# Performance work log

Hardware: AMD Instinct MI355X
Metric: run time of the kernel (lower is better)

## Reference

```python
import jax, jax.numpy as jnp
import numpy as np
from jax import lax

B, L = 2, 5000            # images, candidate lines per image
C_IN, C_LOI = 256, 128    # backbone channels, dim_loi
H = W = 256               # feature-map spatial size (indices clamped to 255)
N_PTS0, N_PTS1 = 32, 8    # points sampled per line, after maxpool
POOL = N_PTS0 // N_PTS1   # MaxPool1d kernel/stride = 4
PLANES = C_LOI // 2       # Bottleneck1D mid channels
EPS = 1e-5


def setup_inputs() -> dict:
    key = jax.random.key(0)
    ks = jax.random.split(key, 16)
    f32 = jnp.float32
    s = 0.05
    feature = jax.random.normal(ks[0], (B, C_IN, H, W), f32)
    lines = jax.random.uniform(ks[1], (B, L, 2, 2), f32, minval=0.0, maxval=255.0)
    return {
        "feature": feature,
        "lines": lines,
        "fc1_w": jax.random.normal(ks[2], (C_LOI, C_IN), f32) * s,
        "fc1_b": jnp.zeros((C_LOI,), f32),
        "bn1_g": jnp.ones((C_LOI,), f32),
        "bn1_b": jnp.zeros((C_LOI,), f32),
        "bn1_m": jax.random.normal(ks[3], (C_LOI,), f32) * 0.1,
        "bn1_v": jax.random.uniform(ks[4], (C_LOI,), f32, minval=0.5, maxval=1.5),
        "conv1_w": jax.random.normal(ks[5], (PLANES, C_LOI), f32) * s,
        "conv1_b": jnp.zeros((PLANES,), f32),
        "bn2_g": jnp.ones((PLANES,), f32),
        "bn2_b": jnp.zeros((PLANES,), f32),
        "bn2_m": jax.random.normal(ks[6], (PLANES,), f32) * 0.1,
        "bn2_v": jax.random.uniform(ks[7], (PLANES,), f32, minval=0.5, maxval=1.5),
        "conv2_w": jax.random.normal(ks[8], (PLANES, PLANES, 3), f32) * s,
        "conv2_b": jnp.zeros((PLANES,), f32),
        "bn3_g": jnp.ones((PLANES,), f32),
        "bn3_b": jnp.zeros((PLANES,), f32),
        "bn3_m": jax.random.normal(ks[9], (PLANES,), f32) * 0.1,
        "bn3_v": jax.random.uniform(ks[10], (PLANES,), f32, minval=0.5, maxval=1.5),
        "conv3_w": jax.random.normal(ks[11], (C_LOI, PLANES), f32) * s,
        "conv3_b": jnp.zeros((C_LOI,), f32),
        "fc2_w": jax.random.normal(ks[12], (3, C_LOI * N_PTS1), f32) * s,
        "fc2_b": jnp.zeros((3,), f32),
    }


def _bn(x, g, b, m, v):
    # eval-mode BatchNorm1d over [N, C, T]
    inv = g / jnp.sqrt(v + EPS)
    return x * inv[None, :, None] + (b - m * inv)[None, :, None]


def _bilinear_sample(feat, lines):
    # feat: [B, C, H, W], lines: [B, L, 2, 2] -> [B, L, C, N_PTS0]
    lam = jnp.linspace(0.0, 1.0, N_PTS0, dtype=feat.dtype)[:, None]  # [P,1]
    # p = lam * endpoint0 + (1-lam) * endpoint1 - 0.5  -> [B, L, P, 2]
    p = lines[:, :, 0:1, :] * lam + lines[:, :, 1:2, :] * (1.0 - lam) - 0.5
    px, py = p[..., 0], p[..., 1]                       # [B, L, P]
    px0 = jnp.clip(jnp.floor(px), 0.0, 255.0)
    py0 = jnp.clip(jnp.floor(py), 0.0, 255.0)
    px1 = jnp.clip(px0 + 1.0, 0.0, 255.0)
    py1 = jnp.clip(py0 + 1.0, 0.0, 255.0)
    ix0, iy0 = px0.astype(jnp.int32), py0.astype(jnp.int32)
    ix1, iy1 = px1.astype(jnp.int32), py1.astype(jnp.int32)
    w00 = (px1 - px) * (py1 - py)
    w10 = (px - px0) * (py1 - py)
    w01 = (px1 - px) * (py - py0)
    w11 = (px - px0) * (py - py0)

    def one_image(f, a0, b0, a1, b1, c00, c10, c01, c11):
        # f: [C,H,W], indices/weights: [L,P] -> [C,L,P]
        return (f[:, a0, b0] * c00 + f[:, a1, b0] * c10 +
                f[:, a0, b1] * c01 + f[:, a1, b1] * c11)

    xp = jax.vmap(one_image)(feat, ix0, iy0, ix1, iy1, w00, w10, w01, w11)
    return jnp.transpose(xp, (0, 2, 1, 3))  # [B, L, C, P]


def _forward(feature, lines, fc1_w, fc1_b, bn1_g, bn1_b, bn1_m, bn1_v,
             conv1_w, conv1_b, bn2_g, bn2_b, bn2_m, bn2_v,
             conv2_w, conv2_b, bn3_g, bn3_b, bn3_m, bn3_v,
             conv3_w, conv3_b, fc2_w, fc2_b):
    # fc1: 1x1 conv over the backbone feature map
    x = jnp.einsum('oc,bchw->bohw', fc1_w, feature) + fc1_b[None, :, None, None]
    xp = _bilinear_sample(x, lines)                     # [B, L, C_LOI, P]
    xp = xp.reshape(B * L, C_LOI, N_PTS0)
    # MaxPool1d(kernel=POOL, stride=POOL)
    xp = xp.reshape(B * L, C_LOI, N_PTS1, POOL).max(axis=-1)  # [N, C, T]
    # Bottleneck1D residual branch: BN-ReLU-Conv1(k1)-BN-ReLU-Conv(k3)-BN-ReLU-Conv(k1)
    h = jax.nn.relu(_bn(xp, bn1_g, bn1_b, bn1_m, bn1_v))
    h = jnp.einsum('oc,nct->not', conv1_w, h) + conv1_b[None, :, None]
    h = jax.nn.relu(_bn(h, bn2_g, bn2_b, bn2_m, bn2_v))
    h = lax.conv_general_dilated(h, conv2_w, window_strides=(1,),
                                 padding=((1, 1),),
                                 dimension_numbers=('NCH', 'OIH', 'NCH'))
    h = h + conv2_b[None, :, None]
    h = jax.nn.relu(_bn(h, bn3_g, bn3_b, bn3_m, bn3_v))
    h = jnp.einsum('oc,nct->not', conv3_w, h) + conv3_b[None, :, None]
    xp = xp + h
    # fc2: ReLU + Linear(dim_loi * n_pts1 -> 3)
    flat = jax.nn.relu(xp).reshape(B * L, C_LOI * N_PTS1)
    return flat @ fc2_w.T + fc2_b


def reference(feature, lines, fc1_w, fc1_b, bn1_g, bn1_b, bn1_m, bn1_v,
              conv1_w, conv1_b, bn2_g, bn2_b, bn2_m, bn2_v,
              conv2_w, conv2_b, bn3_g, bn3_b, bn3_m, bn3_v,
              conv3_w, conv3_b, fc2_w, fc2_b):
    return _forward(feature, lines, fc1_w, fc1_b, bn1_g, bn1_b, bn1_m, bn1_v,
                    conv1_w, conv1_b, bn2_g, bn2_b, bn2_m, bn2_v,
                    conv2_w, conv2_b, bn3_g, bn3_b, bn3_m, bn3_v,
                    conv3_w, conv3_b, fc2_w, fc2_b)
```

## Files before the change

kernel.cpp:

```cpp
#include <hip/hip_runtime.h>
#include <hip/hip_bf16.h>

#define BB 2
#define LL 5000
#define CIN 256
#define CLOI 128
#define HH 256
#define WW 256
#define HWP (HH*WW)
#define NPTS0 32
#define NPTS1 8
#define PLANES 64
#define EPSV 1e-5f

#define X_BYTES   ((size_t)BB * HWP * CLOI * 2)
#define XS_BYTES  ((size_t)BB * LL * 1024 * 2)
#define W1S_OFF   (X_BYTES + XS_BYTES)
#define W2S_OFF   (W1S_OFF + 16384)
#define W3S_OFF   (W2S_OFF + 24576)
#define B1P_OFF   (W3S_OFF + 16384)
#define B2P_OFF   (B1P_OFF + 256)
#define S1_OFF    (B2P_OFF + 256)
#define T1_OFF    (S1_OFF + 512)
#define W0S_OFF   (T1_OFF + 512)

typedef unsigned int uint;
typedef unsigned short ushort;
typedef __attribute__((ext_vector_type(8))) short short8;
typedef __attribute__((ext_vector_type(4))) float f32x4;

__device__ __forceinline__ float bf2f(ushort u) {
    uint v = ((uint)u) << 16;
    return __uint_as_float(v);
}
__device__ __forceinline__ ushort f2bf(float f) {
    uint x = __float_as_uint(f);
    uint r = (x + 0x7fffu + ((x >> 16) & 1u)) >> 16;
    return (ushort)r;
}
__device__ __forceinline__ uint pack2(float a, float b) {
    return (uint)f2bf(a) | ((uint)f2bf(b) << 16);
}

__global__ __launch_bounds__(256) void fc1_kernel(
    const float* __restrict__ feature, const ushort* __restrict__ w0s,
    const float* __restrict__ fc1_b, ushort* __restrict__ xout)
{
    __shared__ ushort sF[32 * 64 * 8];

    int tid = threadIdx.x;
    int tile = blockIdx.x;
    int b = tile >> 10;
    int p0 = (tile & 1023) << 6;
    int wv = tid >> 6, lane = tid & 63;
    int q = lane >> 4, ln = lane & 15;

    short8 afr[8][2];
#pragma unroll
    for (int kg = 0; kg < 8; kg++)
#pragma unroll
        for (int mt = 0; mt < 2; mt++)
            afr[kg][mt] = *(const short8*)(w0s + ((size_t)((kg * 4 + q) * 128 + wv * 32 + mt * 16 + ln)) * 8);

    const float* fb = feature + (size_t)b * CIN * HWP + p0;
    int g_ = tid >> 4;
    int qd = tid & 15;
#pragma unroll
    for (int s = 0; s < 2; s++) {
        int g = s * 16 + g_;
        const float* src = fb + (size_t)(g * 8) * HWP + qd * 4;
        float4 rv[8];
#pragma unroll
        for (int j = 0; j < 8; j++) rv[j] = *(const float4*)(src + (size_t)j * HWP);
#pragma unroll
        for (int i = 0; i < 4; i++) {
            uint4 u;
            u.x = pack2(((const float*)&rv[0])[i], ((const float*)&rv[1])[i]);
            u.y = pack2(((const float*)&rv[2])[i], ((const float*)&rv[3])[i]);
            u.z = pack2(((const float*)&rv[4])[i], ((const float*)&rv[5])[i]);
            u.w = pack2(((const float*)&rv[6])[i], ((const float*)&rv[7])[i]);
            *(uint4*)(&sF[(g * 64 + qd * 4 + i) * 8]) = u;
        }
    }
    __syncthreads();

    const f32x4 fzero = { 0.f, 0.f, 0.f, 0.f };
    f32x4 acc[2][4];
#pragma unroll
    for (int mt = 0; mt < 2; mt++)
#pragma unroll
        for (int nt = 0; nt < 4; nt++) acc[mt][nt] = fzero;

#pragma unroll
    for (int kg = 0; kg < 8; kg++) {
#pragma unroll
        for (int nt = 0; nt < 4; nt++) {
            short8 bfr = *(short8*)(&sF[((kg * 4 + q) * 64 + nt * 16 + ln) * 8]);
            acc[0][nt] = __builtin_amdgcn_mfma_f32_16x16x32_bf16(afr[kg][0], bfr, acc[0][nt], 0, 0, 0);
            acc[1][nt] = __builtin_amdgcn_mfma_f32_16x16x32_bf16(afr[kg][1], bfr, acc[1][nt], 0, 0, 0);
        }
    }

    float bias[8];
    *(float4*)bias       = *(const float4*)(fc1_b + wv * 32 + q * 4);
    *(float4*)(bias + 4) = *(const float4*)(fc1_b + wv * 32 + 16 + q * 4);
    ushort* xrow = xout + (size_t)b * HWP * CLOI;
#pragma unroll
    for (int mt = 0; mt < 2; mt++)
#pragma unroll
        for (int nt = 0; nt < 4; nt++) {
            uint2 u;
            u.x = pack2(acc[mt][nt][0] + bias[mt * 4 + 0], acc[mt][nt][1] + bias[mt * 4 + 1]);
            u.y = pack2(acc[mt][nt][2] + bias[mt * 4 + 2], acc[mt][nt][3] + bias[mt * 4 + 3]);
            *(uint2*)(xrow + (size_t)(p0 + nt * 16 + ln) * CLOI + wv * 32 + mt * 16 + q * 4) = u;
        }
}

__global__ __launch_bounds__(256) void prep_kernel(
    const float* __restrict__ conv1_w, const float* __restrict__ conv1_b,
    const float* __restrict__ bn2_g, const float* __restrict__ bn2_b,
    const float* __restrict__ bn2_m, const float* __restrict__ bn2_v,
    const float* __restrict__ conv2_w, const float* __restrict__ conv2_b,
    const float* __restrict__ bn3_g, const float* __restrict__ bn3_b,
    const float* __restrict__ bn3_m, const float* __restrict__ bn3_v,
    const float* __restrict__ conv3_w,
    const float* __restrict__ bn1_g, const float* __restrict__ bn1_b,
    const float* __restrict__ bn1_m, const float* __restrict__ bn1_v,
    const float* __restrict__ fc1_w,
    ushort* __restrict__ w1s, ushort* __restrict__ w2s, ushort* __restrict__ w3s,
    float* __restrict__ b1p, float* __restrict__ b2p,
    float* __restrict__ s1o, float* __restrict__ t1o,
    ushort* __restrict__ w0s)
{
    int idx = blockIdx.x * 256 + threadIdx.x;
    if (idx < 8192) {
        int kg = idx >> 9, rem = idx & 511, m = rem >> 3, j = rem & 7;
        int c = kg * 8 + j;
        float s2 = bn2_g[m] * rsqrtf(bn2_v[m] + EPSV);
        w1s[idx] = f2bf(conv1_w[m * 128 + c] * s2);
    }
    if (idx < 12288) {
        int dt = idx >> 12, rem = idx & 4095;
        int kg = rem >> 9, m = (rem >> 3) & 63, j = rem & 7;
        int i = kg * 8 + j;
        float s3 = bn3_g[m] * rsqrtf(bn3_v[m] + EPSV);
        w2s[idx] = f2bf(conv2_w[m * 192 + i * 3 + dt] * s3);
    }
    if (idx < 8192) {
        int kg = idx >> 10, rem = idx & 1023, m = rem >> 3, j = rem & 7;
        w3s[idx] = f2bf(conv3_w[m * 64 + kg * 8 + j]);
    }
    if (idx < 32768) {
        int grp = idx >> 10, rem = idx & 1023, m = rem >> 3, j = rem & 7;
        w0s[idx] = f2bf(fc1_w[m * CIN + grp * 8 + j]);
    }
    if (idx < 64) {
        float s2 = bn2_g[idx] * rsqrtf(bn2_v[idx] + EPSV);
        b1p[idx] = conv1_b[idx] * s2 + bn2_b[idx] - bn2_m[idx] * s2;
        float s3 = bn3_g[idx] * rsqrtf(bn3_v[idx] + EPSV);
        b2p[idx] = conv2_b[idx] * s3 + bn3_b[idx] - bn3_m[idx] * s3;
    }
    if (idx < 128) {
        float s1 = bn1_g[idx] * rsqrtf(bn1_v[idx] + EPSV);
        s1o[idx] = s1;
        t1o[idx] = bn1_b[idx] - bn1_m[idx] * s1;
    }
}

__global__ __launch_bounds__(256) void sample_kernel(
    const ushort* __restrict__ x, const float* __restrict__ lines,
    ushort* __restrict__ xsb)
{
    __shared__ int   sIdx[NPTS0][4];
    __shared__ float sWt[NPTS0][4];

    int n = blockIdx.x;
    int b = n / LL;
    int tid = threadIdx.x;

    if (tid < NPTS0) {
        int j = tid;
        float lam = (float)j * (1.0f / 31.0f);
        const float* lp = lines + (size_t)n * 4;
        float e0x = lp[0], e0y = lp[1], e1x = lp[2], e1y = lp[3];
        float px = e0x * lam + e1x * (1.f - lam) - 0.5f;
        float py = e0y * lam + e1y * (1.f - lam) - 0.5f;
        float px0 = fminf(fmaxf(floorf(px), 0.f), 255.f);
        float py0 = fminf(fmaxf(floorf(py), 0.f), 255.f);
        float px1 = fminf(px0 + 1.f, 255.f);
        float py1 = fminf(py0 + 1.f, 255.f);
        int ix0 = (int)px0, iy0 = (int)py0, ix1 = (int)px1, iy1 = (int)py1;
        sIdx[j][0] = ix0 * WW + iy0;
        sIdx[j][1] = ix1 * WW + iy0;
        sIdx[j][2] = ix0 * WW + iy1;
        sIdx[j][3] = ix1 * WW + iy1;
        sWt[j][0] = (px1 - px) * (py1 - py);
        sWt[j][1] = (px - px0) * (py1 - py);
        sWt[j][2] = (px1 - px) * (py - py0);
        sWt[j][3] = (px - px0) * (py - py0);
    }
    __syncthreads();

    int w = tid >> 6, lane = tid & 63;
    const uint* xb = (const uint*)(x + (size_t)b * HWP * CLOI);

    float m00 = -INFINITY, m10 = -INFINITY;
    float m01 = -INFINITY, m11 = -INFINITY;

#pragma unroll
    for (int jj = 0; jj < 8; jj++) {
        int j = w * 8 + jj;
        int i00 = sIdx[j][0], i10 = sIdx[j][1], i01 = sIdx[j][2], i11 = sIdx[j][3];
        float w00 = sWt[j][0], w10 = sWt[j][1], w01 = sWt[j][2], w11 = sWt[j][3];
        uint u00 = xb[(size_t)i00 * 64 + lane];
        uint u10 = xb[(size_t)i10 * 64 + lane];
        uint u01 = xb[(size_t)i01 * 64 + lane];
        uint u11 = xb[(size_t)i11 * 64 + lane];
        float v0 = bf2f((ushort)(u00 & 0xffff)) * w00 + bf2f((ushort)(u10 & 0xffff)) * w10
                 + bf2f((ushort)(u01 & 0xffff)) * w01 + bf2f((ushort)(u11 & 0xffff)) * w11;
        float v1 = bf2f((ushort)(u00 >> 16)) * w00 + bf2f((ushort)(u10 >> 16)) * w10
                 + bf2f((ushort)(u01 >> 16)) * w01 + bf2f((ushort)(u11 >> 16)) * w11;
        if (jj < 4) { m00 = fmaxf(m00, v0); m10 = fmaxf(m10, v1); }
        else        { m01 = fmaxf(m01, v0); m11 = fmaxf(m11, v1); }
    }

    ushort* basep = xsb + (size_t)n * 1024;
    int kg = lane >> 2;
    int j2 = (lane & 3) * 2;
    *(uint*)(basep + kg * 64 + (2 * w) * 8 + j2) = pack2(m00, m10);
    *(uint*)(basep + kg * 64 + (2 * w + 1) * 8 + j2) = pack2(m01, m11);
}

__global__ __launch_bounds__(256) void head_kernel(
    const ushort* __restrict__ xsb,
    const ushort* __restrict__ w1s, const ushort* __restrict__ w2s,
    const ushort* __restrict__ w3s,
    const float* __restrict__ b1p, const float* __restrict__ b2p,
    const float* __restrict__ s1g, const float* __restrict__ t1g,
    const float* __restrict__ conv3_b,
    const float* __restrict__ fc2_w, const float* __restrict__ fc2_b,
    float* __restrict__ out)
{
    __shared__ ushort sXS[8192];
    __shared__ ushort sH1[8192];
    __shared__ ushort sB2[4096];
    __shared__ float  sFC2[3072];
    __shared__ float  sS1[128], sT1[128];
    __shared__ float  sB1[64], sB2b[64], sB3b[128];

    int tid = threadIdx.x;
    int wv = tid >> 6, lane = tid & 63;
    int q = lane >> 4, ln = lane & 15;
    int L0 = blockIdx.x * 8;
    int colg = wv * 16 + ln;

    if (tid < 128) { sS1[tid] = s1g[tid]; sT1[tid] = t1g[tid]; sB3b[tid] = conv3_b[tid]; }
    if (tid < 64)  { sB1[tid] = b1p[tid]; sB2b[tid] = b2p[tid]; }
#pragma unroll
    for (int it = 0; it < 12; it++) sFC2[it * 256 + tid] = fc2_w[it * 256 + tid];
    __syncthreads();

#pragma unroll
    for (int it = 0; it < 4; it++) {
        int ch = it * 256 + tid;
        int l = ch >> 7, wc = ch & 127;
        int kg = wc >> 3, tt = wc & 7;
        int col = l * 8 + tt;
        uint4 raw = *(const uint4*)(xsb + (size_t)(L0 + l) * 1024 + wc * 8);
        int off = (kg * 64 + col) * 8;
        *(uint4*)(&sXS[off]) = raw;
        uint rw[4] = { raw.x, raw.y, raw.z, raw.w };
        uint hw[4];
#pragma unroll
        for (int p = 0; p < 4; p++) {
            int c = kg * 8 + p * 2;
            float v0 = bf2f((ushort)(rw[p] & 0xffff));
            float v1 = bf2f((ushort)(rw[p] >> 16));
            float h0 = fmaxf(v0 * sS1[c] + sT1[c], 0.f);
            float h1v = fmaxf(v1 * sS1[c + 1] + sT1[c + 1], 0.f);
            hw[p] = pack2(h0, h1v);
        }
        uint4 hv; hv.x = hw[0]; hv.y = hw[1]; hv.z = hw[2]; hv.w = hw[3];
        *(uint4*)(&sH1[off]) = hv;
    }
    __syncthreads();

    const short8 bzero = { 0, 0, 0, 0, 0, 0, 0, 0 };
    const f32x4 fzero = { 0.f, 0.f, 0.f, 0.f };

    f32x4 acc1[4];
#pragma unroll
    for (int mt = 0; mt < 4; mt++) acc1[mt] = fzero;
#pragma unroll
    for (int ks = 0; ks < 4; ks++) {
        short8 b = *(short8*)(&sH1[((ks * 4 + q) * 64 + colg) * 8]);
#pragma unroll
        for (int mt = 0; mt < 4; mt++) {
            short8 a = *(const short8*)(w1s + ((ks * 4 + q) * 64 + mt * 16 + ln) * 8);
            acc1[mt] = __builtin_amdgcn_mfma_f32_16x16x32_bf16(a, b, acc1[mt], 0, 0, 0);
        }
    }
#pragma unroll
    for (int mt = 0; mt < 4; mt++) {
        int m0 = mt * 16 + q * 4;
        float v0 = fmaxf(acc1[mt][0] + sB1[m0 + 0], 0.f);
        float v1 = fmaxf(acc1[mt][1] + sB1[m0 + 1], 0.f);
        float v2 = fmaxf(acc1[mt][2] + sB1[m0 + 2], 0.f);
        float v3 = fmaxf(acc1[mt][3] + sB1[m0 + 3], 0.f);
        uint2 u; u.x = pack2(v0, v1); u.y = pack2(v2, v3);
        *(uint2*)(&sB2[((m0 >> 3) * 64 + colg) * 8 + (m0 & 7)]) = u;
    }
    __syncthreads();

    f32x4 acc2[4];
#pragma unroll
    for (int mt = 0; mt < 4; mt++) acc2[mt] = fzero;
    int tpos = colg & 7;
#pragma unroll
    for (int dt = 0; dt < 3; dt++) {
        int tsh = tpos + dt - 1;
        bool valid = ((unsigned)tsh < 8u);
        int colr = colg + dt - 1;
        colr = colr < 0 ? 0 : (colr > 63 ? 63 : colr);
#pragma unroll
        for (int ks = 0; ks < 2; ks++) {
            short8 b = *(short8*)(&sB2[((ks * 4 + q) * 64 + colr) * 8]);
            b = valid ? b : bzero;
#pragma unroll
            for (int mt = 0; mt < 4; mt++) {
                short8 a = *(const short8*)(w2s + dt * 4096 + ((ks * 4 + q) * 64 + mt * 16 + ln) * 8);
                acc2[mt] = __builtin_amdgcn_mfma_f32_16x16x32_bf16(a, b, acc2[mt], 0, 0, 0);
            }
        }
    }
#pragma unroll
    for (int mt = 0; mt < 4; mt++) {
        int m0 = mt * 16 + q * 4;
        float v0 = fmaxf(acc2[mt][0] + sB2b[m0 + 0], 0.f);
        float v1 = fmaxf(acc2[mt][1] + sB2b[m0 + 1], 0.f);
        float v2 = fmaxf(acc2[mt][2] + sB2b[m0 + 2], 0.f);
        float v3 = fmaxf(acc2[mt][3] + sB2b[m0 + 3], 0.f);
        uint2 u; u.x = pack2(v0, v1); u.y = pack2(v2, v3);
        *(uint2*)(&sH1[((m0 >> 3) * 64 + colg) * 8 + (m0 & 7)]) = u;
    }
    __syncthreads();

    f32x4 acc3[8];
#pragma unroll
    for (int mt = 0; mt < 8; mt++) acc3[mt] = fzero;
#pragma unroll
    for (int ks = 0; ks < 2; ks++) {
        short8 b = *(short8*)(&sH1[((ks * 4 + q) * 64 + colg) * 8]);
#pragma unroll
        for (int mt = 0; mt < 8; mt++) {
            short8 a = *(const short8*)(w3s + ((ks * 4 + q) * 128 + mt * 16 + ln) * 8);
            acc3[mt] = __builtin_amdgcn_mfma_f32_16x16x32_bf16(a, b, acc3[mt], 0, 0, 0);
        }
    }

    float p0 = 0.f, p1 = 0.f, p2 = 0.f;
#pragma unroll
    for (int mt = 0; mt < 8; mt++) {
#pragma unroll
        for (int r = 0; r < 4; r++) {
            int m = mt * 16 + q * 4 + r;
            float xsv = bf2f(sXS[(m >> 3) * 512 + colg * 8 + (m & 7)]);
            float v = fmaxf(xsv + acc3[mt][r] + sB3b[m], 0.f);
            int fi = m * 8 + tpos;
            p0 += v * sFC2[fi];
            p1 += v * sFC2[1024 + fi];
            p2 += v * sFC2[2048 + fi];
        }
    }
    p0 += __shfl_xor(p0, 32); p1 += __shfl_xor(p1, 32); p2 += __shfl_xor(p2, 32);
    p0 += __shfl_xor(p0, 16); p1 += __shfl_xor(p1, 16); p2 += __shfl_xor(p2, 16);
    p0 += __shfl_xor(p0, 4);  p1 += __shfl_xor(p1, 4);  p2 += __shfl_xor(p2, 4);
    p0 += __shfl_xor(p0, 2);  p1 += __shfl_xor(p1, 2);  p2 += __shfl_xor(p2, 2);
    p0 += __shfl_xor(p0, 1);  p1 += __shfl_xor(p1, 1);  p2 += __shfl_xor(p2, 1);

    if (lane == 0 || lane == 8) {
        int line = L0 + wv * 2 + (lane >> 3);
        out[(size_t)line * 3 + 0] = p0 + fc2_b[0];
        out[(size_t)line * 3 + 1] = p1 + fc2_b[1];
        out[(size_t)line * 3 + 2] = p2 + fc2_b[2];
    }
}

extern "C" void kernel_launch(void* const* d_in, const int* in_sizes, int n_in,
                              void* d_out, int out_size, void* d_ws, size_t ws_size,
                              hipStream_t stream) {
    const float* feature = (const float*)d_in[0];
    const float* lines   = (const float*)d_in[1];
    const float* fc1_w   = (const float*)d_in[2];
    const float* fc1_b   = (const float*)d_in[3];
    const float* bn1_g   = (const float*)d_in[4];
    const float* bn1_b   = (const float*)d_in[5];
    const float* bn1_m   = (const float*)d_in[6];
    const float* bn1_v   = (const float*)d_in[7];
    const float* conv1_w = (const float*)d_in[8];
    const float* conv1_b = (const float*)d_in[9];
    const float* bn2_g   = (const float*)d_in[10];
    const float* bn2_b   = (const float*)d_in[11];
    const float* bn2_m   = (const float*)d_in[12];
    const float* bn2_v   = (const float*)d_in[13];
    const float* conv2_w = (const float*)d_in[14];
    const float* conv2_b = (const float*)d_in[15];
    const float* bn3_g   = (const float*)d_in[16];
    const float* bn3_b   = (const float*)d_in[17];
    const float* bn3_m   = (const float*)d_in[18];
    const float* bn3_v   = (const float*)d_in[19];
    const float* conv3_w = (const float*)d_in[20];
    const float* conv3_b = (const float*)d_in[21];
    const float* fc2_w   = (const float*)d_in[22];
    const float* fc2_b   = (const float*)d_in[23];
    float* out = (float*)d_out;

    char* ws = (char*)d_ws;
    ushort* x_bf = (ushort*)ws;
    ushort* xs_b = (ushort*)(ws + X_BYTES);
    ushort* w1s  = (ushort*)(ws + W1S_OFF);
    ushort* w2s  = (ushort*)(ws + W2S_OFF);
    ushort* w3s  = (ushort*)(ws + W3S_OFF);
    float*  b1p  = (float*)(ws + B1P_OFF);
    float*  b2p  = (float*)(ws + B2P_OFF);
    float*  s1g  = (float*)(ws + S1_OFF);
    float*  t1g  = (float*)(ws + T1_OFF);
    ushort* w0s  = (ushort*)(ws + W0S_OFF);

    prep_kernel<<<128, 256, 0, stream>>>(
        conv1_w, conv1_b, bn2_g, bn2_b, bn2_m, bn2_v,
        conv2_w, conv2_b, bn3_g, bn3_b, bn3_m, bn3_v,
        conv3_w, bn1_g, bn1_b, bn1_m, bn1_v, fc1_w,
        w1s, w2s, w3s, b1p, b2p, s1g, t1g, w0s);
    fc1_kernel<<<2048, 256, 0, stream>>>(feature, w0s, fc1_b, x_bf);
    sample_kernel<<<BB * LL, 256, 0, stream>>>(x_bf, lines, xs_b);
    head_kernel<<<BB * LL / 8, 256, 0, stream>>>(
        xs_b, w1s, w2s, w3s, b1p, b2p, s1g, t1g, conv3_b, fc2_w, fc2_b, out);
}
```

Baseline: 299.3 us.

## Vectorize bilinear gathers, use hardware bf16 packing, drop fc2 LDS staging

```diff
diff --git a/kernel.cpp b/kernel.cpp
--- a/kernel.cpp
+++ b/kernel.cpp
@@ -29,17 +29,20 @@
 typedef __attribute__((ext_vector_type(8))) short short8;
 typedef __attribute__((ext_vector_type(4))) float f32x4;
 
-__device__ __forceinline__ float bf2f(ushort u) {
-    uint v = ((uint)u) << 16;
-    return __uint_as_float(v);
-}
+__device__ __forceinline__ float bfLow(uint u)  { return __uint_as_float(u << 16); }
+__device__ __forceinline__ float bfHigh(uint u) { return __uint_as_float(u & 0xffff0000u); }
+__device__ __forceinline__ float bf2f(ushort u) { return __uint_as_float(((uint)u) << 16); }
 __device__ __forceinline__ ushort f2bf(float f) {
     uint x = __float_as_uint(f);
     uint r = (x + 0x7fffu + ((x >> 16) & 1u)) >> 16;
     return (ushort)r;
 }
-__device__ __forceinline__ uint pack2(float a, float b) {
-    return (uint)f2bf(a) | ((uint)f2bf(b) << 16);
+__device__ __forceinline__ uint pk2(float a, float b) {
+    float2 f; f.x = a; f.y = b;
+    __hip_bfloat162 h = __float22bfloat162_rn(f);
+    uint r;
+    __builtin_memcpy(&r, &h, 4);
+    return r;
 }
 
 __global__ __launch_bounds__(256) void fc1_kernel(
@@ -75,10 +78,10 @@
 #pragma unroll
         for (int i = 0; i < 4; i++) {
             uint4 u;
-            u.x = pack2(((const float*)&rv[0])[i], ((const float*)&rv[1])[i]);
-            u.y = pack2(((const float*)&rv[2])[i], ((const float*)&rv[3])[i]);
-            u.z = pack2(((const float*)&rv[4])[i], ((const float*)&rv[5])[i]);
-            u.w = pack2(((const float*)&rv[6])[i], ((const float*)&rv[7])[i]);
+            u.x = pk2(((const float*)&rv[0])[i], ((const float*)&rv[1])[i]);
+            u.y = pk2(((const float*)&rv[2])[i], ((const float*)&rv[3])[i]);
+            u.z = pk2(((const float*)&rv[4])[i], ((const float*)&rv[5])[i]);
+            u.w = pk2(((const float*)&rv[6])[i], ((const float*)&rv[7])[i]);
             *(uint4*)(&sF[(g * 64 + qd * 4 + i) * 8]) = u;
         }
     }
@@ -110,8 +113,8 @@
 #pragma unroll
         for (int nt = 0; nt < 4; nt++) {
             uint2 u;
-            u.x = pack2(acc[mt][nt][0] + bias[mt * 4 + 0], acc[mt][nt][1] + bias[mt * 4 + 1]);
-            u.y = pack2(acc[mt][nt][2] + bias[mt * 4 + 2], acc[mt][nt][3] + bias[mt * 4 + 3]);
+            u.x = pk2(acc[mt][nt][0] + bias[mt * 4 + 0], acc[mt][nt][1] + bias[mt * 4 + 1]);
+            u.y = pk2(acc[mt][nt][2] + bias[mt * 4 + 2], acc[mt][nt][3] + bias[mt * 4 + 3]);
             *(uint2*)(xrow + (size_t)(p0 + nt * 16 + ln) * CLOI + wv * 32 + mt * 16 + q * 4) = u;
         }
 }
@@ -171,8 +174,8 @@
     const ushort* __restrict__ x, const float* __restrict__ lines,
     ushort* __restrict__ xsb)
 {
-    __shared__ int   sIdx[NPTS0][4];
-    __shared__ float sWt[NPTS0][4];
+    __shared__ int    sBase[NPTS0];
+    __shared__ float4 sW4[NPTS0];
 
     int n = blockIdx.x;
     int b = n / LL;
@@ -187,48 +190,57 @@
         float py = e0y * lam + e1y * (1.f - lam) - 0.5f;
         float px0 = fminf(fmaxf(floorf(px), 0.f), 255.f);
         float py0 = fminf(fmaxf(floorf(py), 0.f), 255.f);
-        float px1 = fminf(px0 + 1.f, 255.f);
-        float py1 = fminf(py0 + 1.f, 255.f);
-        int ix0 = (int)px0, iy0 = (int)py0, ix1 = (int)px1, iy1 = (int)py1;
-        sIdx[j][0] = ix0 * WW + iy0;
-        sIdx[j][1] = ix1 * WW + iy0;
-        sIdx[j][2] = ix0 * WW + iy1;
-        sIdx[j][3] = ix1 * WW + iy1;
-        sWt[j][0] = (px1 - px) * (py1 - py);
-        sWt[j][1] = (px - px0) * (py1 - py);
-        sWt[j][2] = (px1 - px) * (py - py0);
-        sWt[j][3] = (px - px0) * (py - py0);
-    }
-    __syncthreads();
-
-    int w = tid >> 6, lane = tid & 63;
-    const uint* xb = (const uint*)(x + (size_t)b * HWP * CLOI);
-
-    float m00 = -INFINITY, m10 = -INFINITY;
-    float m01 = -INFINITY, m11 = -INFINITY;
+        float px1 = px0 + 1.f;
+        float py1 = py0 + 1.f;
+        int ix0 = (int)px0, iy0 = (int)py0;
+        sBase[j] = (ix0 * WW + iy0) * 256;
+        float4 w;
+        w.x = (px1 - px) * (py1 - py);
+        w.y = (px - px0) * (py1 - py);
+        w.z = (px1 - px) * (py - py0);
+        w.w = (px - px0) * (py - py0);
+        sW4[j] = w;
+    }
+    __syncthreads();
+
+    int wv = tid >> 6, lane = tid & 63;
+    bool hiHalf = lane >= 32;
+    int loff = lane * 8;
+    const char* xbc = (const char*)(x + (size_t)b * HWP * CLOI);
+
+    float m0 = -INFINITY, m1 = -INFINITY, m2 = -INFINITY, m3 = -INFINITY;
 
 #pragma unroll
     for (int jj = 0; jj < 8; jj++) {
-        int j = w * 8 + jj;
-        int i00 = sIdx[j][0], i10 = sIdx[j][1], i01 = sIdx[j][2], i11 = sIdx[j][3];
-        float w00 = sWt[j][0], w10 = sWt[j][1], w01 = sWt[j][2], w11 = sWt[j][3];
-        uint u00 = xb[(size_t)i00 * 64 + lane];
-        uint u10 = xb[(size_t)i10 * 64 + lane];
-        uint u01 = xb[(size_t)i01 * 64 + lane];
-        uint u11 = xb[(size_t)i11 * 64 + lane];
-        float v0 = bf2f((ushort)(u00 & 0xffff)) * w00 + bf2f((ushort)(u10 & 0xffff)) * w10
-                 + bf2f((ushort)(u01 & 0xffff)) * w01 + bf2f((ushort)(u11 & 0xffff)) * w11;
-        float v1 = bf2f((ushort)(u00 >> 16)) * w00 + bf2f((ushort)(u10 >> 16)) * w10
-                 + bf2f((ushort)(u01 >> 16)) * w01 + bf2f((ushort)(u11 >> 16)) * w11;
-        if (jj < 4) { m00 = fmaxf(m00, v0); m10 = fmaxf(m10, v1); }
-        else        { m01 = fmaxf(m01, v0); m11 = fmaxf(m11, v1); }
-    }
-
-    ushort* basep = xsb + (size_t)n * 1024;
-    int kg = lane >> 2;
-    int j2 = (lane & 3) * 2;
-    *(uint*)(basep + kg * 64 + (2 * w) * 8 + j2) = pack2(m00, m10);
-    *(uint*)(basep + kg * 64 + (2 * w + 1) * 8 + j2) = pack2(m01, m11);
+        int j = wv * 8 + jj;
+        int b0 = sBase[j];
+        float4 w4 = sW4[j];
+        int rb0 = __builtin_amdgcn_readfirstlane(b0);
+        const char* pA = xbc + rb0;
+        const char* pB = pA + 65536;
+        uint2 l1 = *(const uint2*)(pA + loff);
+        uint2 l2 = *(const uint2*)(pB + loff);
+        float wA = hiHalf ? w4.z : w4.x;
+        float wB = hiHalf ? w4.w : w4.y;
+        float t0 = bfLow(l1.x) * wA + bfLow(l2.x) * wB;
+        float t1 = bfHigh(l1.x) * wA + bfHigh(l2.x) * wB;
+        float t2 = bfLow(l1.y) * wA + bfLow(l2.y) * wB;
+        float t3 = bfHigh(l1.y) * wA + bfHigh(l2.y) * wB;
+        t0 += __shfl_xor(t0, 32);
+        t1 += __shfl_xor(t1, 32);
+        t2 += __shfl_xor(t2, 32);
+        t3 += __shfl_xor(t3, 32);
+        if ((jj >= 4) == hiHalf) {
+            m0 = fmaxf(m0, t0); m1 = fmaxf(m1, t1);
+            m2 = fmaxf(m2, t2); m3 = fmaxf(m3, t3);
+        }
+    }
+
+    int t = 2 * wv + (hiHalf ? 1 : 0);
+    int c0 = (lane & 31) * 4;
+    int kg = c0 >> 3;
+    uint2 u; u.x = pk2(m0, m1); u.y = pk2(m2, m3);
+    *(uint2*)(xsb + (size_t)n * 1024 + kg * 64 + t * 8 + (c0 & 7)) = u;
 }
 
 __global__ __launch_bounds__(256) void head_kernel(
@@ -244,7 +256,6 @@
     __shared__ ushort sXS[8192];
     __shared__ ushort sH1[8192];
     __shared__ ushort sB2[4096];
-    __shared__ float  sFC2[3072];
     __shared__ float  sS1[128], sT1[128];
     __shared__ float  sB1[64], sB2b[64], sB3b[128];
 
@@ -256,8 +267,6 @@
 
     if (tid < 128) { sS1[tid] = s1g[tid]; sT1[tid] = t1g[tid]; sB3b[tid] = conv3_b[tid]; }
     if (tid < 64)  { sB1[tid] = b1p[tid]; sB2b[tid] = b2p[tid]; }
-#pragma unroll
-    for (int it = 0; it < 12; it++) sFC2[it * 256 + tid] = fc2_w[it * 256 + tid];
     __syncthreads();
 
 #pragma unroll
@@ -274,11 +283,9 @@
 #pragma unroll
         for (int p = 0; p < 4; p++) {
             int c = kg * 8 + p * 2;
-            float v0 = bf2f((ushort)(rw[p] & 0xffff));
-            float v1 = bf2f((ushort)(rw[p] >> 16));
-            float h0 = fmaxf(v0 * sS1[c] + sT1[c], 0.f);
-            float h1v = fmaxf(v1 * sS1[c + 1] + sT1[c + 1], 0.f);
-            hw[p] = pack2(h0, h1v);
+            float h0  = fmaxf(bfLow(rw[p])  * sS1[c]     + sT1[c],     0.f);
+            float h1v = fmaxf(bfHigh(rw[p]) * sS1[c + 1] + sT1[c + 1], 0.f);
+            hw[p] = pk2(h0, h1v);
         }
         uint4 hv; hv.x = hw[0]; hv.y = hw[1]; hv.z = hw[2]; hv.w = hw[3];
         *(uint4*)(&sH1[off]) = hv;
@@ -307,7 +314,7 @@
         float v1 = fmaxf(acc1[mt][1] + sB1[m0 + 1], 0.f);
         float v2 = fmaxf(acc1[mt][2] + sB1[m0 + 2], 0.f);
         float v3 = fmaxf(acc1[mt][3] + sB1[m0 + 3], 0.f);
-        uint2 u; u.x = pack2(v0, v1); u.y = pack2(v2, v3);
+        uint2 u; u.x = pk2(v0, v1); u.y = pk2(v2, v3);
         *(uint2*)(&sB2[((m0 >> 3) * 64 + colg) * 8 + (m0 & 7)]) = u;
     }
     __syncthreads();
@@ -340,7 +347,7 @@
         float v1 = fmaxf(acc2[mt][1] + sB2b[m0 + 1], 0.f);
         float v2 = fmaxf(acc2[mt][2] + sB2b[m0 + 2], 0.f);
         float v3 = fmaxf(acc2[mt][3] + sB2b[m0 + 3], 0.f);
-        uint2 u; u.x = pack2(v0, v1); u.y = pack2(v2, v3);
+        uint2 u; u.x = pk2(v0, v1); u.y = pk2(v2, v3);
         *(uint2*)(&sH1[((m0 >> 3) * 64 + colg) * 8 + (m0 & 7)]) = u;
     }
     __syncthreads();
@@ -361,15 +368,18 @@
     float p0 = 0.f, p1 = 0.f, p2 = 0.f;
 #pragma unroll
     for (int mt = 0; mt < 8; mt++) {
+        int m0 = mt * 16 + q * 4;
+        int kg = m0 >> 3;
+        uint2 xr = *(uint2*)(&sXS[kg * 512 + colg * 8 + (m0 & 7)]);
+        float xsv[4] = { bfLow(xr.x), bfHigh(xr.x), bfLow(xr.y), bfHigh(xr.y) };
 #pragma unroll
         for (int r = 0; r < 4; r++) {
-            int m = mt * 16 + q * 4 + r;
-            float xsv = bf2f(sXS[(m >> 3) * 512 + colg * 8 + (m & 7)]);
-            float v = fmaxf(xsv + acc3[mt][r] + sB3b[m], 0.f);
+            int m = m0 + r;
+            float v = fmaxf(xsv[r] + acc3[mt][r] + sB3b[m], 0.f);
             int fi = m * 8 + tpos;
-            p0 += v * sFC2[fi];
-            p1 += v * sFC2[1024 + fi];
-            p2 += v * sFC2[2048 + fi];
+            p0 += v * fc2_w[fi];
+            p1 += v * fc2_w[1024 + fi];
+            p2 += v * fc2_w[2048 + fi];
         }
     }
     p0 += __shfl_xor(p0, 32); p1 += __shfl_xor(p1, 32); p2 += __shfl_xor(p2, 32);
```

Result: no change. 300.1 us (+0.3%).
